# Kernel tuning notes

Hardware: AMD Instinct MI355X
Metric: run time of the kernel (lower is better)

Reference implementation:

```python
import jax, jax.numpy as jnp
import numpy as np

NUM_EMBEDDINGS = 512
EMBEDDING_DIM = 128
COMMITMENT_COST = 0.6
MID_HR = 100.0
HR_RANGE = 70.0


def setup_inputs() -> dict:
    key = jax.random.key(0)
    k1, k2 = jax.random.split(key)
    inputs = jax.random.normal(k1, (64, 2048, EMBEDDING_DIM), dtype=jnp.float32)
    # torch init: uniform(-1/K, 1/K)
    emb_weight = jax.random.uniform(
        k2, (NUM_EMBEDDINGS, EMBEDDING_DIM), dtype=jnp.float32,
        minval=-1.0 / NUM_EMBEDDINGS, maxval=1.0 / NUM_EMBEDDINGS)
    scaling = jnp.ones((NUM_EMBEDDINGS,), dtype=jnp.float32)
    return {"inputs": inputs, "emb_weight": emb_weight, "scaling": scaling}


def reference(inputs, emb_weight, scaling):
    B, T, D = inputs.shape
    K = emb_weight.shape[0]
    flat = inputs.reshape(-1, D)  # [N, D]
    # squared L2 distances to all codes: [N, K]
    distances = (
        jnp.sum(flat * flat, axis=1, keepdims=True)
        + jnp.sum(emb_weight * emb_weight, axis=1)
        - 2.0 * flat @ emb_weight.T
    )
    hr_values = jnp.linspace(40.0, 180.0, K, dtype=jnp.float32)
    hr_weights = 1.0 + scaling * ((hr_values - MID_HR) / HR_RANGE)  # [K]
    encoding_indices = jnp.argmin(distances * hr_weights[None, :], axis=1)  # [N]
    # one-hot @ codebook == direct gather
    quantized = emb_weight[encoding_indices].reshape(inputs.shape)
    e_latent_loss = jnp.mean((jax.lax.stop_gradient(quantized) - inputs) ** 2)
    q_latent_loss = jnp.mean((quantized - jax.lax.stop_gradient(inputs)) ** 2)
    loss = q_latent_loss + COMMITMENT_COST * e_latent_loss
    # straight-through estimator
    quantized_st = inputs + jax.lax.stop_gradient(quantized - inputs)
    return quantized_st, loss, encoding_indices.reshape(B, T)
```

## Files before the change

kernel.cpp:

```cpp
#include <hip/hip_runtime.h>

#define NCODES 512
#define DIM 128
#define NROWS (64*2048)
#define QN (NROWS*DIM)
#define BLK_ROWS 512
#define NBLOCKS (NROWS/BLK_ROWS)
#define NWAVES 16

typedef __attribute__((ext_vector_type(8))) short short8;
typedef __attribute__((ext_vector_type(4))) float f32x4;

__device__ __forceinline__ unsigned short f2bf(float f) {
  unsigned u = __builtin_bit_cast(unsigned, f);
  u += 0x7FFFu + ((u >> 16) & 1u);
  return (unsigned short)(u >> 16);
}

#define GLOAD_LDS16(gp, lp) __builtin_amdgcn_global_load_lds( \
    (__attribute__((address_space(1))) void*)(gp), \
    (__attribute__((address_space(3))) void*)(lp), 16, 0, 0)

__global__ void vq_prep(const float* __restrict__ emb, const float* __restrict__ scaling,
                        unsigned short* __restrict__ emb_bf,
                        float* __restrict__ wv, float* __restrict__ wse,
                        float* __restrict__ wrcp) {
  int k = blockIdx.x;
  int l = threadIdx.x;
  float2 v = ((const float2*)(emb + k * DIM))[l];
  float ss = v.x * v.x + v.y * v.y;
#pragma unroll
  for (int m = 1; m < 64; m <<= 1) ss += __shfl_xor(ss, m);
  unsigned pack = (unsigned)f2bf(v.x) | ((unsigned)f2bf(v.y) << 16);
  ((unsigned*)emb_bf)[k * 64 + l] = pack;
  if (l == 0) {
    float hr = 40.0f + (float)k * (140.0f / 511.0f);
    float wt = 1.0f + scaling[k] * ((hr - 100.0f) * (1.0f / 70.0f));
    wv[k] = wt;
    wse[k] = wt * ss;
    wrcp[k] = 1.0f / wt;
  }
}

struct SmemT {
  unsigned short frag[NCODES * DIM];
  float w[NCODES];
  float wse[NCODES];
  float wrcp[NCODES];
};

__global__ __launch_bounds__(1024, 4) void vq_main(
    const float* __restrict__ x,
    const float* __restrict__ emb32,
    const unsigned short* __restrict__ emb_bf,
    const float* __restrict__ wv,
    const float* __restrict__ wse,
    const float* __restrict__ wrcp,
    float* __restrict__ out_q,
    float* __restrict__ out_idx,
    float* __restrict__ partials) {
  __shared__ SmemT sm;
  const int tid = threadIdx.x;
  const int wave = tid >> 6, lane = tid & 63;
  const int g = lane >> 4, lr = lane & 15;
  const long rowbase = (long)blockIdx.x * BLK_ROWS + wave * 32;

  float4 xv[2][4][2];
#pragma unroll
  for (int rg = 0; rg < 2; rg++) {
    const float* xr = x + (rowbase + rg * 16 + lr) * DIM + g * 8;
#pragma unroll
    for (int c = 0; c < 4; c++) {
      xv[rg][c][0] = *(const float4*)(xr + c * 32);
      xv[rg][c][1] = *(const float4*)(xr + c * 32 + 4);
    }
  }

  {
    const uint4* src = (const uint4*)emb_bf;
#pragma unroll
    for (int i = 0; i < 8; i++) {
      int winst = wave * 8 + i;
      int d = winst * 64 + lane;
      int t = d >> 8, c = (d >> 6) & 3, gg = (d >> 4) & 3, rr = d & 15;
      int s = (t * 16 + rr) * 16 + c * 4 + gg;
      GLOAD_LDS16(src + s, (char*)sm.frag + winst * 1024);
    }
    if (tid < NCODES) {
      sm.w[tid] = wv[tid];
      sm.wse[tid] = wse[tid];
      sm.wrcp[tid] = wrcp[tid];
    }
  }

  short8 a[2][4];
  float sr[2][4];
  {
    float srow[2];
#pragma unroll
    for (int rg = 0; rg < 2; rg++) {
      float ss = 0.f;
#pragma unroll
      for (int c = 0; c < 4; c++) {
        float4 v0 = xv[rg][c][0];
        float4 v1 = xv[rg][c][1];
        ss += v0.x * v0.x + v0.y * v0.y + v0.z * v0.z + v0.w * v0.w;
        ss += v1.x * v1.x + v1.y * v1.y + v1.z * v1.z + v1.w * v1.w;
        short8 av;
        av[0] = (short)f2bf(v0.x); av[1] = (short)f2bf(v0.y);
        av[2] = (short)f2bf(v0.z); av[3] = (short)f2bf(v0.w);
        av[4] = (short)f2bf(v1.x); av[5] = (short)f2bf(v1.y);
        av[6] = (short)f2bf(v1.z); av[7] = (short)f2bf(v1.w);
        a[rg][c] = av;
      }
      ss += __shfl_xor(ss, 16);
      ss += __shfl_xor(ss, 32);
      srow[rg] = ss;
    }
#pragma unroll
    for (int rg = 0; rg < 2; rg++)
#pragma unroll
      for (int r = 0; r < 4; r++)
        sr[rg][r] = __shfl(srow[rg], g * 4 + r);
  }
  __syncthreads();

  float vmin[2][4];
  int imin[2][4];
#pragma unroll
  for (int rg = 0; rg < 2; rg++)
#pragma unroll
    for (int r = 0; r < 4; r++) { vmin[rg][r] = 3.0e38f; imin[rg][r] = 0; }

  const short8* __restrict__ bbase = (const short8*)sm.frag + lane;
  for (int t = 0; t < 32; t++) {
    const int code = t * 16 + lr;
    const float wt = sm.w[code];
    const float bb = sm.wse[code];
    const float m2w = -2.0f * wt;
    f32x4 acc0 = {0.f, 0.f, 0.f, 0.f};
    f32x4 acc1 = {0.f, 0.f, 0.f, 0.f};
#pragma unroll
    for (int c = 0; c < 4; c++) {
      short8 bf = bbase[(t * 4 + c) * 64];
      acc0 = __builtin_amdgcn_mfma_f32_16x16x32_bf16(a[0][c], bf, acc0, 0, 0, 0);
      acc1 = __builtin_amdgcn_mfma_f32_16x16x32_bf16(a[1][c], bf, acc1, 0, 0, 0);
    }
#pragma unroll
    for (int r = 0; r < 4; r++) {
      float v0 = fmaf(m2w, acc0[r], fmaf(wt, sr[0][r], bb));
      float v1 = fmaf(m2w, acc1[r], fmaf(wt, sr[1][r], bb));
      if (v0 < vmin[0][r]) { vmin[0][r] = v0; imin[0][r] = code; }
      if (v1 < vmin[1][r]) { vmin[1][r] = v1; imin[1][r] = code; }
    }
  }

#pragma unroll
  for (int m = 1; m <= 8; m <<= 1) {
#pragma unroll
    for (int rg = 0; rg < 2; rg++)
#pragma unroll
      for (int r = 0; r < 4; r++) {
        float ov = __shfl_xor(vmin[rg][r], m);
        int oi = __shfl_xor(imin[rg][r], m);
        if (ov < vmin[rg][r] || (ov == vmin[rg][r] && oi < imin[rg][r])) {
          vmin[rg][r] = ov; imin[rg][r] = oi;
        }
      }
  }

  {
    float l0 = 0.f;
#pragma unroll
    for (int rg = 0; rg < 2; rg++)
#pragma unroll
      for (int r = 0; r < 4; r++) {
        int ci = imin[rg][r];
        l0 = fmaf(vmin[rg][r], sm.wrcp[ci], l0);
        if (lr == 0) out_idx[rowbase + rg * 16 + g * 4 + r] = (float)ci;
      }
    l0 += __shfl_xor(l0, 16);
    l0 += __shfl_xor(l0, 32);
    if (lane == 0) partials[blockIdx.x * NWAVES + wave] = l0;
  }

  {
    const uint4* __restrict__ esrc = (const uint4*)emb32;
    uint4* __restrict__ outu = (uint4*)out_q + rowbase * 32;
    const int col = lane & 31;
    const int hi = lane >> 5;
#pragma unroll
    for (int it = 0; it < 16; it++) {
      const int row0 = 2 * it;
      const int rg = row0 >> 4;
      const int gn = (row0 >> 2) & 3;
      const int r0 = row0 & 3;
      int c0 = __shfl(imin[rg][r0], gn * 16);
      int c1 = __shfl(imin[rg][r0 + 1], gn * 16);
      int code = hi ? c1 : c0;
      outu[it * 64 + lane] = esrc[code * 32 + col];
    }
  }
}

__global__ void vq_loss(const float* __restrict__ partials, float* __restrict__ out_loss) {
  __shared__ float red[16];
  const int t = threadIdx.x;
  float s = 0.f;
  for (int i = t; i < NBLOCKS * NWAVES; i += 1024) s += partials[i];
#pragma unroll
  for (int m = 1; m < 64; m <<= 1) s += __shfl_xor(s, m);
  if ((t & 63) == 0) red[t >> 6] = s;
  __syncthreads();
  if (t == 0) {
    float tot = 0.f;
    for (int i = 0; i < 16; i++) tot += red[i];
    out_loss[0] = tot * (1.6f / (float)QN);
  }
}

extern "C" void kernel_launch(void* const* d_in, const int* in_sizes, int n_in,
                              void* d_out, int out_size, void* d_ws, size_t ws_size,
                              hipStream_t stream) {
  const float* x = (const float*)d_in[0];
  const float* emb = (const float*)d_in[1];
  const float* scaling = (const float*)d_in[2];

  float* out_q = (float*)d_out;
  float* out_loss = out_q + QN;
  float* out_idx = out_q + QN + 1;

  unsigned short* emb_bf = (unsigned short*)d_ws;
  float* wv = (float*)((char*)d_ws + NCODES * DIM * 2);
  float* wse = wv + NCODES;
  float* wrcp = wse + NCODES;
  float* partials = wrcp + NCODES;

  vq_prep<<<NCODES, 64, 0, stream>>>(emb, scaling, emb_bf, wv, wse, wrcp);
  vq_main<<<NBLOCKS, 1024, 0, stream>>>(x, emb, emb_bf, wv, wse, wrcp,
                                        out_q, out_idx, partials);
  vq_loss<<<1, 1024, 0, stream>>>(partials, out_loss);
}
```

Measured before the change: 50.11 us.

## Fuse loss reduction into main kernel via atomics and batch gather loads

Removes the separate single-block loss-reduction kernel. Each block now reduces its per-wave loss partials in shared memory and atomically adds the scaled sum into the output, with a memset to zero it first. The codebook gather for the quantized output is split into batches of eight loads followed by eight stores to raise memory-level parallelism, and the distance loop is unrolled by two. The atomic accumulation makes the summation order nondeterministic, and the memset is one more operation on the stream.

```diff
diff --git a/kernel.cpp b/kernel.cpp
--- a/kernel.cpp
+++ b/kernel.cpp
@@ -47,6 +47,7 @@
   float w[NCODES];
   float wse[NCODES];
   float wrcp[NCODES];
+  float lossp[NWAVES];
 };
 
 __global__ __launch_bounds__(1024, 4) void vq_main(
@@ -58,7 +59,7 @@
     const float* __restrict__ wrcp,
     float* __restrict__ out_q,
     float* __restrict__ out_idx,
-    float* __restrict__ partials) {
+    float* __restrict__ out_loss) {
   __shared__ SmemT sm;
   const int tid = threadIdx.x;
   const int wave = tid >> 6, lane = tid & 63;
@@ -133,6 +134,7 @@
     for (int r = 0; r < 4; r++) { vmin[rg][r] = 3.0e38f; imin[rg][r] = 0; }
 
   const short8* __restrict__ bbase = (const short8*)sm.frag + lane;
+#pragma unroll 2
   for (int t = 0; t < 32; t++) {
     const int code = t * 16 + lr;
     const float wt = sm.w[code];
@@ -181,7 +183,7 @@
       }
     l0 += __shfl_xor(l0, 16);
     l0 += __shfl_xor(l0, 32);
-    if (lane == 0) partials[blockIdx.x * NWAVES + wave] = l0;
+    if (lane == 0) sm.lossp[wave] = l0;
   }
 
   {
@@ -189,6 +191,7 @@
     uint4* __restrict__ outu = (uint4*)out_q + rowbase * 32;
     const int col = lane & 31;
     const int hi = lane >> 5;
+    int scode[16];
 #pragma unroll
     for (int it = 0; it < 16; it++) {
       const int row0 = 2 * it;
@@ -197,25 +200,26 @@
       const int r0 = row0 & 3;
       int c0 = __shfl(imin[rg][r0], gn * 16);
       int c1 = __shfl(imin[rg][r0 + 1], gn * 16);
-      int code = hi ? c1 : c0;
-      outu[it * 64 + lane] = esrc[code * 32 + col];
-    }
-  }
-}
-
-__global__ void vq_loss(const float* __restrict__ partials, float* __restrict__ out_loss) {
-  __shared__ float red[16];
-  const int t = threadIdx.x;
-  float s = 0.f;
-  for (int i = t; i < NBLOCKS * NWAVES; i += 1024) s += partials[i];
-#pragma unroll
-  for (int m = 1; m < 64; m <<= 1) s += __shfl_xor(s, m);
-  if ((t & 63) == 0) red[t >> 6] = s;
+      scode[it] = hi ? c1 : c0;
+    }
+#pragma unroll
+    for (int half = 0; half < 2; half++) {
+      uint4 vbuf[8];
+#pragma unroll
+      for (int j = 0; j < 8; j++)
+        vbuf[j] = esrc[scode[half * 8 + j] * 32 + col];
+#pragma unroll
+      for (int j = 0; j < 8; j++)
+        outu[(half * 8 + j) * 64 + lane] = vbuf[j];
+    }
+  }
+
   __syncthreads();
-  if (t == 0) {
-    float tot = 0.f;
-    for (int i = 0; i < 16; i++) tot += red[i];
-    out_loss[0] = tot * (1.6f / (float)QN);
+  if (wave == 0 && lane < NWAVES) {
+    float s = sm.lossp[lane];
+#pragma unroll
+    for (int m = 1; m < NWAVES; m <<= 1) s += __shfl_xor(s, m);
+    if (lane == 0) atomicAdd(out_loss, s * (1.6f / (float)QN));
   }
 }
 
@@ -234,10 +238,9 @@
   float* wv = (float*)((char*)d_ws + NCODES * DIM * 2);
   float* wse = wv + NCODES;
   float* wrcp = wse + NCODES;
-  float* partials = wrcp + NCODES;
-
+
+  hipMemsetAsync(out_loss, 0, sizeof(float), stream);
   vq_prep<<<NCODES, 64, 0, stream>>>(emb, scaling, emb_bf, wv, wse, wrcp);
   vq_main<<<NBLOCKS, 1024, 0, stream>>>(x, emb, emb_bf, wv, wse, wrcp,
-                                        out_q, out_idx, partials);
-  vq_loss<<<1, 1024, 0, stream>>>(partials, out_loss);
-}
+                                        out_q, out_idx, out_loss);
+}
```

After: 51.82 us. 3.4% more time.
